# Optimization experiments

Hardware: AMD Instinct MI355X
Metric: run time of the kernel (lower is better)

## Reference

```python
import jax, jax.numpy as jnp
import numpy as np

# config: image_scale = (depth, height, width), landmarkNum, sigma
D, H, W = 96, 96, 96
N_LANDMARKS = 19
BATCH = 4
SIGMA = 2.0


def setup_inputs() -> dict:
    key = jax.random.key(0)
    k1, k2 = jax.random.split(key)
    predicted_heatmap = jax.random.normal(k1, (BATCH, N_LANDMARKS, D, H, W), dtype=jnp.float32)
    # normalized coords in [0,1) -> all landmarks valid (>= 0)
    labels = jax.random.uniform(k2, (BATCH, N_LANDMARKS, 3), dtype=jnp.float32)
    return {"predicted_heatmap": predicted_heatmap, "labels": labels}


def _generate_target_heatmap(labels_pixel):
    # labels_pixel: (B, N, 3) in pixel space (x->W, y->H, z->D)
    gz = jnp.arange(D, dtype=jnp.float32)[:, None, None]   # (D,1,1)
    gh = jnp.arange(H, dtype=jnp.float32)[None, :, None]   # (1,H,1)
    gw = jnp.arange(W, dtype=jnp.float32)[None, None, :]   # (1,1,W)
    x = labels_pixel[..., 0][..., None, None, None]  # (B,N,1,1,1)
    y = labels_pixel[..., 1][..., None, None, None]
    z = labels_pixel[..., 2][..., None, None, None]
    dist_sq = (gw - x) ** 2 + (gh - y) ** 2 + (gz - z) ** 2  # (B,N,D,H,W)
    hm = jnp.exp(-dist_sq / (2.0 * SIGMA ** 2))
    s = hm.sum(axis=(-3, -2, -1), keepdims=True)
    hm = jnp.where(s > 0, hm / s, hm)  # normalize to sum 1 (guard s==0)
    valid = (labels_pixel[..., 0] >= 0)[..., None, None, None]
    return jnp.where(valid, hm, jnp.zeros((), dtype=hm.dtype))


def reference(predicted_heatmap, labels):
    # predicted_heatmap: (B, N, D, H, W) == torch.stack(list_of_(B,D,H,W), dim=1)
    scale = jnp.array([W - 1, H - 1, D - 1], dtype=jnp.float32)
    labels_pixel = labels * scale
    target = jax.lax.stop_gradient(_generate_target_heatmap(labels_pixel))
    mask = (labels[:, :, 0] >= 0).astype(jnp.float32)[:, :, None, None, None]  # (B,N,1,1,1)
    loss = jnp.abs(predicted_heatmap - target)
    total_loss = (loss * mask).sum()
    valid_points_count = mask.sum() + 1e-8
    return total_loss / valid_points_count
```

## Files before the change

kernel.cpp:

```cpp
#include <hip/hip_runtime.h>

#define DD 96
#define HH 96
#define WW 96
#define BN 76
#define SLICE4 (HH*WW/4)
#define W4R (WW/4)
#define NSLICE (BN*DD)
#define NT 384

__global__ void __launch_bounds__(NT) loss_kernel(
        const float*  __restrict__ labels,
        const float4* __restrict__ pred,
        float* __restrict__ part) {
    const int bx  = blockIdx.x;
    const int bn  = bx / DD;
    const int d   = bx - bn * DD;
    const int tid = threadIdx.x;

    __shared__ __align__(16) float ew_s[96];
    __shared__ float eh_s[96];
    __shared__ float ed_s[96];
    __shared__ float fh_s[96];
    __shared__ float sums_s[3];
    __shared__ float wsum[NT / 64];

    const float lx = labels[bn * 3 + 0];
    const float ly = labels[bn * 3 + 1];
    const float lz = labels[bn * 3 + 2];
    const float x = lx * 95.0f;
    const float y = ly * 95.0f;
    const float z = lz * 95.0f;

    if (tid < 96) {
        const float fi = (float)tid;
        const float dx = fi - x, dy = fi - y, dz = fi - z;
        ew_s[tid] = __expf(-dx * dx * 0.125f);
        eh_s[tid] = __expf(-dy * dy * 0.125f);
        ed_s[tid] = __expf(-dz * dz * 0.125f);
    }
    __syncthreads();

    if (tid < 64) {
        float a = ew_s[tid], b = eh_s[tid], c = ed_s[tid];
        if (tid < 32) { a += ew_s[tid + 64]; b += eh_s[tid + 64]; c += ed_s[tid + 64]; }
        for (int off = 32; off > 0; off >>= 1) {
            a += __shfl_down(a, off, 64);
            b += __shfl_down(b, off, 64);
            c += __shfl_down(c, off, 64);
        }
        if (tid == 0) { sums_s[0] = a; sums_s[1] = b; sums_s[2] = c; }
    }
    __syncthreads();

    const float s   = sums_s[0] * sums_s[1] * sums_s[2];
    const float inv = (s > 0.0f) ? (1.0f / s) : 1.0f;
    if (tid < 96) fh_s[tid] = eh_s[tid] * (ed_s[d] * inv);
    __syncthreads();

    const int w4 = tid % W4R;
    const float4 e = reinterpret_cast<const float4*>(ew_s)[w4];

    const float4* p0 = pred + (size_t)bx * SLICE4;
    float acc = 0.0f;
    #pragma unroll
    for (int k = 0; k < 6; ++k) {
        const int t = tid + k * NT;
        const float4 p = p0[t];
        const float  f = fh_s[t / W4R];
        acc += fabsf(p.x - e.x * f) + fabsf(p.y - e.y * f)
             + fabsf(p.z - e.z * f) + fabsf(p.w - e.w * f);
    }
    acc *= (lx >= 0.0f) ? 1.0f : 0.0f;

    for (int off = 32; off > 0; off >>= 1)
        acc += __shfl_down(acc, off, 64);
    const int lane = tid & 63;
    const int wid  = tid >> 6;
    if (lane == 0) wsum[wid] = acc;
    __syncthreads();
    if (tid == 0) {
        float t2 = 0.0f;
        #pragma unroll
        for (int i = 0; i < NT / 64; ++i) t2 += wsum[i];
        part[bx] = t2;
    }
}

__global__ void __launch_bounds__(256) finalize_kernel(
        const float* __restrict__ part,
        const float* __restrict__ labels,
        float* __restrict__ out) {
    const int tid = threadIdx.x;

    float acc = 0.0f;
    for (int i = tid; i < NSLICE; i += 256) acc += part[i];
    float cnt = (tid < BN) ? ((labels[tid * 3] >= 0.0f) ? 1.0f : 0.0f) : 0.0f;

    for (int off = 32; off > 0; off >>= 1) {
        acc += __shfl_down(acc, off, 64);
        cnt += __shfl_down(cnt, off, 64);
    }
    __shared__ float wsA[4], wsC[4];
    const int lane = tid & 63;
    const int wid  = tid >> 6;
    if (lane == 0) { wsA[wid] = acc; wsC[wid] = cnt; }
    __syncthreads();
    if (tid == 0) {
        const float tot = wsA[0] + wsA[1] + wsA[2] + wsA[3];
        const float c   = wsC[0] + wsC[1] + wsC[2] + wsC[3];
        out[0] = tot / (c + 1e-8f);
    }
}

extern "C" void kernel_launch(void* const* d_in, const int* in_sizes, int n_in,
                              void* d_out, int out_size, void* d_ws, size_t ws_size,
                              hipStream_t stream) {
    const float* pred   = (const float*)d_in[0];
    const float* labels = (const float*)d_in[1];
    float* out = (float*)d_out;

    float* part = (float*)d_ws;

    loss_kernel<<<NSLICE, NT, 0, stream>>>(labels, (const float4*)pred, part);
    finalize_kernel<<<1, 256, 0, stream>>>(part, labels, out);
}
```

Baseline: 51.63 us.

## Process six depth slices per block to amortize Gaussian table setup

Each block now covers a group of six consecutive depth slices of one landmark instead of a single slice. The separable Gaussian factors and their normalization are computed once per block, and the per-row height factors are hoisted into registers and scaled by the depth factor inside the loop. This removes repeated exp, reduction and barrier overhead and shrinks the partial-sum array. In exchange there are far fewer blocks, which may reduce latency hiding or cause tail imbalance on a bandwidth-bound streaming kernel.

```diff
diff --git a/kernel.cpp b/kernel.cpp
--- a/kernel.cpp
+++ b/kernel.cpp
@@ -6,7 +6,9 @@
 #define BN 76
 #define SLICE4 (HH*WW/4)
 #define W4R (WW/4)
-#define NSLICE (BN*DD)
+#define DG 6
+#define NGRP (DD/DG)
+#define NBLK (BN*NGRP)
 #define NT 384
 
 __global__ void __launch_bounds__(NT) loss_kernel(
@@ -14,8 +16,8 @@
         const float4* __restrict__ pred,
         float* __restrict__ part) {
     const int bx  = blockIdx.x;
-    const int bn  = bx / DD;
-    const int d   = bx - bn * DD;
+    const int bn  = bx / NGRP;
+    const int d0  = (bx - bn * NGRP) * DG;
     const int tid = threadIdx.x;
 
     __shared__ __align__(16) float ew_s[96];
@@ -55,21 +57,28 @@
 
     const float s   = sums_s[0] * sums_s[1] * sums_s[2];
     const float inv = (s > 0.0f) ? (1.0f / s) : 1.0f;
-    if (tid < 96) fh_s[tid] = eh_s[tid] * (ed_s[d] * inv);
+    if (tid < 96) fh_s[tid] = eh_s[tid] * inv;
     __syncthreads();
 
-    const int w4 = tid % W4R;
+    const int h0 = tid / W4R;
+    const int w4 = tid - h0 * W4R;
     const float4 e = reinterpret_cast<const float4*>(ew_s)[w4];
+    float fhr[6];
+    #pragma unroll
+    for (int k = 0; k < 6; ++k) fhr[k] = fh_s[h0 + 16 * k];
 
-    const float4* p0 = pred + (size_t)bx * SLICE4;
+    const float4* p0 = pred + (size_t)(bn * DD + d0) * SLICE4 + tid;
     float acc = 0.0f;
-    #pragma unroll
-    for (int k = 0; k < 6; ++k) {
-        const int t = tid + k * NT;
-        const float4 p = p0[t];
-        const float  f = fh_s[t / W4R];
-        acc += fabsf(p.x - e.x * f) + fabsf(p.y - e.y * f)
-             + fabsf(p.z - e.z * f) + fabsf(p.w - e.w * f);
+    #pragma unroll 2
+    for (int dd = 0; dd < DG; ++dd) {
+        const float edv = ed_s[d0 + dd];
+        #pragma unroll
+        for (int k = 0; k < 6; ++k) {
+            const float4 p = p0[dd * SLICE4 + k * NT];
+            const float  f = fhr[k] * edv;
+            acc += fabsf(p.x - e.x * f) + fabsf(p.y - e.y * f)
+                 + fabsf(p.z - e.z * f) + fabsf(p.w - e.w * f);
+        }
     }
     acc *= (lx >= 0.0f) ? 1.0f : 0.0f;
 
@@ -94,7 +103,7 @@
     const int tid = threadIdx.x;
 
     float acc = 0.0f;
-    for (int i = tid; i < NSLICE; i += 256) acc += part[i];
+    for (int i = tid; i < NBLK; i += 256) acc += part[i];
     float cnt = (tid < BN) ? ((labels[tid * 3] >= 0.0f) ? 1.0f : 0.0f) : 0.0f;
 
     for (int off = 32; off > 0; off >>= 1) {
@@ -122,6 +131,6 @@
 
     float* part = (float*)d_ws;
 
-    loss_kernel<<<NSLICE, NT, 0, stream>>>(labels, (const float4*)pred, part);
+    loss_kernel<<<NBLK, NT, 0, stream>>>(labels, (const float4*)pred, part);
     finalize_kernel<<<1, 256, 0, stream>>>(part, labels, out);
 }
```

Measured after the change: 46.37 us. 1.11x faster.
